# Kernel optimization log

Measured on AMD Instinct MI355X. Metric: run time of the kernel, lower is better.

## Reference

```python
import jax, jax.numpy as jnp
import numpy as np
import math

B, S, H, D = 8, 4096, 768, 64  # batch, seq_len, hidden_dim, head_size


def setup_inputs() -> dict:
    key = jax.random.key(0)
    kx, kk, kq, kv, kbk, kbq, kbv = jax.random.split(key, 7)
    s = 1.0 / math.sqrt(H)
    return {
        "x": jax.random.normal(kx, (B, S, H), dtype=jnp.float32),
        "Wk": jax.random.normal(kk, (H, D), dtype=jnp.float32) * s,
        "bk": jax.random.normal(kbk, (D,), dtype=jnp.float32) * s,
        "Wq": jax.random.normal(kq, (H, D), dtype=jnp.float32) * s,
        "bq": jax.random.normal(kbq, (D,), dtype=jnp.float32) * s,
        "Wv": jax.random.normal(kv, (H, D), dtype=jnp.float32) * s,
        "bv": jax.random.normal(kbv, (D,), dtype=jnp.float32) * s,
    }


def reference(x, Wk, bk, Wq, bq, Wv, bv):
    # projections: [B, S, D]
    k = x @ Wk + bk
    q = x @ Wq + bq
    v = x @ Wv + bv
    # full O(S^2) attention scores, as in the original module
    weight = jnp.einsum("bqd,bkd->bqk", q, k)  # [B, S, S]
    causal = jnp.tril(jnp.ones((S, S), dtype=bool))
    # original masks first, then divides by sqrt(head_size); -inf/sqrt = -inf
    weight = jnp.where(causal, weight, -jnp.inf) / math.sqrt(D)
    weight = jax.nn.softmax(weight, axis=-1)
    # dropout p=0.0 (eval-mode reference): identity
    out = jnp.einsum("bqk,bkd->bqd", weight, v)  # [B, S, D]
    return out
```

## Files before the change

### kernel.cpp

```cpp
#include <hip/hip_runtime.h>
#include <hip/hip_bf16.h>
#include <math.h>

#define B_ 8
#define S_ 4096
#define H_ 768
#define D_ 64

typedef __bf16 bf16;
typedef bf16 bf16x8 __attribute__((ext_vector_type(8)));
typedef bf16 bf16x4 __attribute__((ext_vector_type(4)));
typedef float floatx4 __attribute__((ext_vector_type(4)));

__device__ __forceinline__ int sw_off(int r, int chunk) {
    return r * 128 + ((chunk ^ (r & 7)) << 4);
}
__device__ __forceinline__ int sw_elem(int r, int e) {
    return r * 64 + (((e >> 3) ^ (r & 7)) << 3) + (e & 7);
}

__device__ __forceinline__ void dma16(const bf16* gsrc, bf16* ldst) {
    __builtin_amdgcn_global_load_lds(
        (const __attribute__((address_space(1))) unsigned int*)(const void*)gsrc,
        (__attribute__((address_space(3))) unsigned int*)(void*)ldst,
        16, 0, 0);
}

__global__ __launch_bounds__(256) void wtrans_kernel(
    const float* __restrict__ Wq, const float* __restrict__ Wk,
    const float* __restrict__ Wv, bf16* __restrict__ wt)
{
    __shared__ bf16 t_lds[64][72];
    const float* W = (blockIdx.y == 0) ? Wq : (blockIdx.y == 1) ? Wk : Wv;
    bf16* o = wt + ((size_t)blockIdx.y * 12 + blockIdx.x) * 4096;
    const int k0 = blockIdx.x * 64;
    const int tid = threadIdx.x;
    #pragma unroll
    for (int rep = 0; rep < 16; ++rep) {
        int idx = rep * 256 + tid;
        int r = idx >> 6, n = idx & 63;
        t_lds[n][r] = (bf16)W[(size_t)(k0 + r) * D_ + n];
    }
    __syncthreads();
    #pragma unroll
    for (int rep = 0; rep < 16; ++rep) {
        int idx = rep * 256 + tid;
        int n = idx >> 6, kk = idx & 63;
        o[sw_elem(n, kk)] = t_lds[n][kk];
    }
}

__global__ __launch_bounds__(256, 2) void proj_kernel(
    const float* __restrict__ x, const bf16* __restrict__ wt,
    const float* __restrict__ bq, const float* __restrict__ bk,
    const float* __restrict__ bv,
    bf16* __restrict__ qout, bf16* __restrict__ kout, bf16* __restrict__ vtt)
{
    __shared__ bf16 wlds[2][3][4096];

    const int m0   = blockIdx.x * 64;
    const int tid  = threadIdx.x;
    const int lane = tid & 63;
    const int wave = tid >> 6;
    const int quad = lane >> 4;
    const int c    = lane & 15;
    const int mrow = m0 + wave * 16 + c;

    floatx4 acc[3][4] = {};
    const float* xrow = &x[(size_t)mrow * H_ + quad * 8];

    auto loadA = [&](int k0, bf16x8* dst) {
        #pragma unroll
        for (int s = 0; s < 2; ++s) {
            const float* xp = xrow + k0 + s * 32;
            float4 f0 = *(const float4*)xp;
            float4 f1 = *(const float4*)(xp + 4);
            bf16x8 a;
            a[0] = (bf16)f0.x; a[1] = (bf16)f0.y; a[2] = (bf16)f0.z; a[3] = (bf16)f0.w;
            a[4] = (bf16)f1.x; a[5] = (bf16)f1.y; a[6] = (bf16)f1.z; a[7] = (bf16)f1.w;
            dst[s] = a;
        }
    };
    auto stageW = [&](int kt, int buf) {
        #pragma unroll
        for (int w = 0; w < 3; ++w) {
            const bf16* src = wt + (size_t)(w * 12 + kt) * 4096 + wave * 1024 + lane * 8;
            bf16* dst = &wlds[buf][w][wave * 1024];
            dma16(src, dst);
            dma16(src + 512, dst + 512);
        }
    };

    bf16x8 afn[2]; loadA(0, afn);
    stageW(0, 0);

    for (int kt = 0; kt < 12; ++kt) {
        __syncthreads();
        const int cur = kt & 1;
        if (kt < 11) stageW(kt + 1, 1 - cur);
        bf16x8 af[2] = { afn[0], afn[1] };
        if (kt < 11) loadA((kt + 1) * 64, afn);
        #pragma unroll
        for (int s = 0; s < 2; ++s)
            #pragma unroll
            for (int w = 0; w < 3; ++w)
                #pragma unroll
                for (int tn = 0; tn < 4; ++tn) {
                    bf16x8 bfrag = *(const bf16x8*)
                        ((const char*)&wlds[cur][w][0] + sw_off(tn * 16 + c, s * 4 + quad));
                    acc[w][tn] = __builtin_amdgcn_mfma_f32_16x16x32_bf16(
                        af[s], bfrag, acc[w][tn], 0, 0, 0);
                }
    }

    const int rbase = m0 + wave * 16 + quad * 4;
    const int bb = m0 >> 12;
    const int jt = (m0 & 4095) >> 6;
    const size_t tbase = ((size_t)bb * 64 + jt) * 4096;
    #pragma unroll
    for (int tn = 0; tn < 4; ++tn) {
        const int n = tn * 16 + c;
        float bqv = bq[n];
        #pragma unroll
        for (int r = 0; r < 4; ++r)
            qout[(size_t)(rbase + r) * 128 + n] = (bf16)(acc[0][tn][r] + bqv);
        float bkv = bk[n];
        #pragma unroll
        for (int r = 0; r < 4; ++r) {
            const int sl = (rbase & 63) + r;
            kout[tbase + sw_elem(sl, n)] = (bf16)(acc[1][tn][r] + bkv);
        }
        float bvv = bv[n];
        bf16x4 pk;
        #pragma unroll
        for (int r = 0; r < 4; ++r) pk[r] = (bf16)(acc[2][tn][r] + bvv);
        const int sl0 = (rbase & 63);
        *(bf16x4*)&vtt[tbase + sw_elem(n, sl0)] = pk;
    }
}

__global__ __launch_bounds__(256, 2) void attn_kernel(
    const bf16* __restrict__ q, const bf16* __restrict__ k,
    const bf16* __restrict__ vt, float* __restrict__ out)
{
    __shared__ bf16 klds[2][4096];
    __shared__ bf16 vlds[2][4096];
    __shared__ bf16 plds[4][16 * 72];

    const int tid  = threadIdx.x;
    const int lane = tid & 63;
    const int wave = tid >> 6;
    const int quad = lane >> 4;
    const int c    = lane & 15;
    const int i    = blockIdx.x;
    const int b    = i & 7;
    const int t    = (i < 256) ? (63 - (i >> 3)) : ((i - 256) >> 3);
    const float cl = 0.18033688011112042f;
    const float M2 = 16.0f;

    const bf16* ktile0 = k  + (size_t)b * 64 * 4096;
    const bf16* vtile0 = vt + (size_t)b * 64 * 4096;
    bf16* pl = &plds[wave][0];

    auto stage = [&](const bf16* gsrc, bf16* ldst) {
        const bf16* s = gsrc + wave * 1024 + lane * 8;
        bf16* d = ldst + wave * 1024;
        dma16(s, d);
        dma16(s + 512, d + 512);
    };

    bf16x8 qf[2];
    #pragma unroll
    for (int s = 0; s < 2; ++s)
        qf[s] = *(const bf16x8*)
            &q[(size_t)(b * S_ + t * 64 + wave * 16 + c) * 128 + s * 32 + quad * 8];

    floatx4 acc_o[4] = {};
    float lpart[4] = {0.f, 0.f, 0.f, 0.f};

    stage(ktile0, klds[0]);
    stage(vtile0, vlds[0]);

    #pragma unroll 1
    for (int j = 0; j <= t; ++j) {
        __syncthreads();
        const int cur = j & 1;
        if (j < t) {
            stage(ktile0 + (size_t)(j + 1) * 4096, klds[1 - cur]);
            stage(vtile0 + (size_t)(j + 1) * 4096, vlds[1 - cur]);
        }

        floatx4 sa[4] = {};
        #pragma unroll
        for (int s = 0; s < 2; ++s)
            #pragma unroll
            for (int tn = 0; tn < 4; ++tn) {
                bf16x8 kf = *(const bf16x8*)
                    ((const char*)&klds[cur][0] + sw_off(tn * 16 + c, s * 4 + quad));
                sa[tn] = __builtin_amdgcn_mfma_f32_16x16x32_bf16(qf[s], kf, sa[tn], 0, 0, 0);
            }

        if (j == t) {
            #pragma unroll
            for (int tn = 0; tn < 4; ++tn) {
                const int col = tn * 16 + c;
                #pragma unroll
                for (int r = 0; r < 4; ++r)
                    if (col > wave * 16 + quad * 4 + r) sa[tn][r] = -INFINITY;
            }
        }

        #pragma unroll
        for (int tn = 0; tn < 4; ++tn)
            #pragma unroll
            for (int r = 0; r < 4; ++r) {
                float p = __builtin_amdgcn_exp2f(fmaf(sa[tn][r], cl, -M2));
                sa[tn][r] = p;
                lpart[r] += p;
            }

        bf16x8 vf[2][4];
        #pragma unroll
        for (int s = 0; s < 2; ++s)
            #pragma unroll
            for (int tn = 0; tn < 4; ++tn)
                vf[s][tn] = *(const bf16x8*)
                    ((const char*)&vlds[cur][0] + sw_off(tn * 16 + c, s * 4 + quad));

        #pragma unroll
        for (int tn = 0; tn < 4; ++tn)
            #pragma unroll
            for (int r = 0; r < 4; ++r)
                pl[(quad * 4 + r) * 72 + tn * 16 + c] = (bf16)sa[tn][r];

        bf16x8 pf[2];
        #pragma unroll
        for (int s = 0; s < 2; ++s)
            pf[s] = *(const bf16x8*)&pl[c * 72 + s * 32 + quad * 8];

        #pragma unroll
        for (int s = 0; s < 2; ++s)
            #pragma unroll
            for (int tn = 0; tn < 4; ++tn)
                acc_o[tn] = __builtin_amdgcn_mfma_f32_16x16x32_bf16(pf[s], vf[s][tn], acc_o[tn], 0, 0, 0);
    }

    #pragma unroll
    for (int r = 0; r < 4; ++r) {
        lpart[r] += __shfl_xor(lpart[r], 1);
        lpart[r] += __shfl_xor(lpart[r], 2);
        lpart[r] += __shfl_xor(lpart[r], 4);
        lpart[r] += __shfl_xor(lpart[r], 8);
    }

    float rl[4];
    #pragma unroll
    for (int r = 0; r < 4; ++r) rl[r] = 1.0f / lpart[r];
    #pragma unroll
    for (int tn = 0; tn < 4; ++tn)
        #pragma unroll
        for (int r = 0; r < 4; ++r)
            out[(size_t)(b * S_ + t * 64 + wave * 16 + quad * 4 + r) * D_ + tn * 16 + c]
                = acc_o[tn][r] * rl[r];
}

extern "C" void kernel_launch(void* const* d_in, const int* in_sizes, int n_in,
                              void* d_out, int out_size, void* d_ws, size_t ws_size,
                              hipStream_t stream) {
    const float* x  = (const float*)d_in[0];
    const float* Wk = (const float*)d_in[1];
    const float* bk = (const float*)d_in[2];
    const float* Wq = (const float*)d_in[3];
    const float* bq = (const float*)d_in[4];
    const float* Wv = (const float*)d_in[5];
    const float* bv = (const float*)d_in[6];
    float* out = (float*)d_out;

    bf16* q_ws  = (bf16*)d_out;
    bf16* k_ws  = (bf16*)d_ws;
    bf16* vt_ws = k_ws + (size_t)B_ * S_ * D_;
    bf16* wt_ws = vt_ws + (size_t)B_ * S_ * D_;

    wtrans_kernel<<<dim3(H_ / 64, 3), 256, 0, stream>>>(Wq, Wk, Wv, wt_ws);
    proj_kernel<<<dim3(B_ * S_ / 64), 256, 0, stream>>>(
        x, wt_ws, bq, bk, bv, q_ws, k_ws, vt_ws);
    attn_kernel<<<dim3(512), 256, 0, stream>>>(q_ws, k_ws, vt_ws, out);
}
```

Before: 232.8 us.

## Split attention into 32-row query tiles with two-wave blocks and swizzled P buffer

The attention kernel now uses 128-thread blocks, each covering 32 query rows instead of 64, and launches 1024 blocks. The block-to-tile mapping interleaves long and short causal rows across four slots for load balance. Each wave stages twice as much K/V per DMA round, and the per-wave P scratch switches from padded rows to an XOR-swizzled layout. The aim is more blocks in flight and less causal waste per block, at the cost of loading each K/V tile twice as often overall.

```diff
diff --git a/kernel.cpp b/kernel.cpp
--- a/kernel.cpp
+++ b/kernel.cpp
@@ -139,13 +139,13 @@
     }
 }
 
-__global__ __launch_bounds__(256, 2) void attn_kernel(
+__global__ __launch_bounds__(128, 2) void attn_kernel(
     const bf16* __restrict__ q, const bf16* __restrict__ k,
     const bf16* __restrict__ vt, float* __restrict__ out)
 {
     __shared__ bf16 klds[2][4096];
     __shared__ bf16 vlds[2][4096];
-    __shared__ bf16 plds[4][16 * 72];
+    __shared__ bf16 plds[2][1024];
 
     const int tid  = threadIdx.x;
     const int lane = tid & 63;
@@ -153,8 +153,14 @@
     const int quad = lane >> 4;
     const int c    = lane & 15;
     const int i    = blockIdx.x;
-    const int b    = i & 7;
-    const int t    = (i < 256) ? (63 - (i >> 3)) : ((i - 256) >> 3);
+    const int slot = i >> 8;
+    const int cc   = i & 255;
+    const int b    = cc & 7;
+    const int x    = cc >> 3;
+    const int qt   = (slot == 0) ? (127 - x) : (slot == 1) ? x
+                   : (slot == 2) ? (95 - x)  : (32 + x);
+    const int jmax = qt >> 1;
+    const int qrow = qt * 32 + wave * 16;
     const float cl = 0.18033688011112042f;
     const float M2 = 16.0f;
 
@@ -163,17 +169,17 @@
     bf16* pl = &plds[wave][0];
 
     auto stage = [&](const bf16* gsrc, bf16* ldst) {
-        const bf16* s = gsrc + wave * 1024 + lane * 8;
-        bf16* d = ldst + wave * 1024;
-        dma16(s, d);
-        dma16(s + 512, d + 512);
+        const bf16* s = gsrc + wave * 2048 + lane * 8;
+        bf16* d = ldst + wave * 2048;
+        #pragma unroll
+        for (int n = 0; n < 4; ++n) dma16(s + n * 512, d + n * 512);
     };
 
     bf16x8 qf[2];
     #pragma unroll
     for (int s = 0; s < 2; ++s)
         qf[s] = *(const bf16x8*)
-            &q[(size_t)(b * S_ + t * 64 + wave * 16 + c) * 128 + s * 32 + quad * 8];
+            &q[(size_t)(b * S_ + qrow + c) * 128 + s * 32 + quad * 8];
 
     floatx4 acc_o[4] = {};
     float lpart[4] = {0.f, 0.f, 0.f, 0.f};
@@ -182,10 +188,10 @@
     stage(vtile0, vlds[0]);
 
     #pragma unroll 1
-    for (int j = 0; j <= t; ++j) {
+    for (int j = 0; j <= jmax; ++j) {
         __syncthreads();
         const int cur = j & 1;
-        if (j < t) {
+        if (j < jmax) {
             stage(ktile0 + (size_t)(j + 1) * 4096, klds[1 - cur]);
             stage(vtile0 + (size_t)(j + 1) * 4096, vlds[1 - cur]);
         }
@@ -200,13 +206,13 @@
                 sa[tn] = __builtin_amdgcn_mfma_f32_16x16x32_bf16(qf[s], kf, sa[tn], 0, 0, 0);
             }
 
-        if (j == t) {
+        if (j == jmax) {
             #pragma unroll
             for (int tn = 0; tn < 4; ++tn) {
-                const int col = tn * 16 + c;
+                const int col = j * 64 + tn * 16 + c;
                 #pragma unroll
                 for (int r = 0; r < 4; ++r)
-                    if (col > wave * 16 + quad * 4 + r) sa[tn][r] = -INFINITY;
+                    if (col > qrow + quad * 4 + r) sa[tn][r] = -INFINITY;
             }
         }
 
@@ -231,12 +237,12 @@
         for (int tn = 0; tn < 4; ++tn)
             #pragma unroll
             for (int r = 0; r < 4; ++r)
-                pl[(quad * 4 + r) * 72 + tn * 16 + c] = (bf16)sa[tn][r];
+                pl[sw_elem(quad * 4 + r, tn * 16 + c)] = (bf16)sa[tn][r];
 
         bf16x8 pf[2];
         #pragma unroll
         for (int s = 0; s < 2; ++s)
-            pf[s] = *(const bf16x8*)&pl[c * 72 + s * 32 + quad * 8];
+            pf[s] = *(const bf16x8*)((const char*)pl + sw_off(c, s * 4 + quad));
 
         #pragma unroll
         for (int s = 0; s < 2; ++s)
@@ -260,7 +266,7 @@
     for (int tn = 0; tn < 4; ++tn)
         #pragma unroll
         for (int r = 0; r < 4; ++r)
-            out[(size_t)(b * S_ + t * 64 + wave * 16 + quad * 4 + r) * D_ + tn * 16 + c]
+            out[(size_t)(b * S_ + qrow + quad * 4 + r) * D_ + tn * 16 + c]
                 = acc_o[tn][r] * rl[r];
 }
 
@@ -284,5 +290,5 @@
     wtrans_kernel<<<dim3(H_ / 64, 3), 256, 0, stream>>>(Wq, Wk, Wv, wt_ws);
     proj_kernel<<<dim3(B_ * S_ / 64), 256, 0, stream>>>(
         x, wt_ws, bq, bk, bv, q_ws, k_ws, vt_ws);
-    attn_kernel<<<dim3(512), 256, 0, stream>>>(q_ws, k_ws, vt_ws, out);
-}
+    attn_kernel<<<dim3(1024), 128, 0, stream>>>(q_ws, k_ws, vt_ws, out);
+}
```

Measured after the change: 232.2 us. Within noise of the previous version (-0.3%).
